# Kernel tuning notes

Hardware: AMD Instinct MI355X
Metric: run time of the kernel (lower is better)

## Reference

```python
import jax, jax.numpy as jnp
import numpy as np

B, FRAMES, NBINS, HOP = 4, 400, 129, 240
T = FRAMES * HOP  # 96000


def hann_window(K, dtype=jnp.float32):
    # torch.hann_window default is periodic=True: 0.5*(1 - cos(2*pi*n/K))
    n = jnp.arange(K, dtype=dtype)
    return 0.5 - 0.5 * jnp.cos(2.0 * jnp.pi * n / K)


def get_minimum_phase_fir(log_mag):
    # log_mag: [B, F, NBINS] -> full spectrum [B, F, N], N = 2*(NBINS-1)
    full = jnp.concatenate([log_mag, jnp.flip(log_mag, -1)[..., 1:-1]], axis=-1)
    N = full.shape[-1]
    # Hilbert transform (scipy-style analytic signal), N even
    Xf = jnp.fft.fft(full, axis=-1)
    h = jnp.concatenate([
        jnp.ones((1,), full.dtype),
        2.0 * jnp.ones((N // 2 - 1,), full.dtype),
        jnp.ones((1,), full.dtype),
        jnp.zeros((N // 2 - 1,), full.dtype),
    ])
    analytic = jnp.fft.ifft(Xf * h, axis=-1)
    min_phase = -jnp.imag(analytic)
    freq_resp = jnp.exp(full + 1j * min_phase)
    return jnp.real(jnp.fft.ifft(freq_resp, axis=-1))  # [B, F, N]


def windowing(kernel):
    K = kernel.shape[-1]
    w = hann_window(K, kernel.dtype)
    w = w.at[: K // 2].set(1.0)
    return kernel * w


def upsample_linear(x, scale):
    # x: [B, K, L] -> [B, K, L*scale], matches F.upsample(mode='linear', align_corners=False)
    L = x.shape[-1]
    out = jnp.arange(L * scale, dtype=x.dtype)
    src = jnp.clip((out + 0.5) / scale - 0.5, 0.0, L - 1.0)
    lo = jnp.floor(src).astype(jnp.int32)
    hi = jnp.minimum(lo + 1, L - 1)
    w = src - lo.astype(x.dtype)
    return x[..., lo] * (1.0 - w) + x[..., hi] * w


def fir_filt(x, h):
    # x: [B, T], h: [B, T, K]; causal time-varying FIR: y[t] = sum_k h[t,k] * x[t-k]
    K = h.shape[-1]
    Tn = x.shape[-1]
    x_pad = jnp.pad(x, ((0, 0), (K - 1, 0)))
    idx = jnp.arange(Tn)[:, None] + jnp.arange(K)[None, :]  # [T, K]
    frames = x_pad[:, idx]  # [B, T, K] (im2col-like gather)
    return jnp.einsum('btk,btk->bt', frames, jnp.flip(h, -1))


def setup_inputs() -> dict:
    key = jax.random.key(0)
    k1, k2 = jax.random.split(key)
    ex = jax.random.normal(k1, (B, T), dtype=jnp.float32)
    log_mag = jax.random.normal(k2, (B, FRAMES, NBINS), dtype=jnp.float32)
    return {"ex": ex, "log_mag": log_mag, "hop_length": HOP}


def reference(ex, log_mag, hop_length):
    kernel = get_minimum_phase_fir(log_mag)          # [B, F, K]
    kernel = windowing(kernel)
    up = upsample_linear(jnp.transpose(kernel, (0, 2, 1)), hop_length)  # [B, K, F*hop]
    up = jnp.transpose(up, (0, 2, 1))                # [B, F*hop, K]
    Tn = min(ex.shape[1], up.shape[1])
    ex = ex[:, :Tn]
    up = up[:, :Tn]
    return fir_filt(ex, up)
```

## Files before the change

kernel.cpp:

```cpp
#include <hip/hip_runtime.h>
#include <math.h>

#define NB 4
#define FRAMES 400
#define NBINS 129
#define HOP 240
#define T_LEN (FRAMES * HOP)
#define KLEN 256

#define REC_C { const float cn = fmaf(a2, cm, -cm1); cm1 = cm; cm = cn; }
#define REC_S { const float sn = fmaf(a2, sm, -sm1); sm1 = sm; sm = sn; }

__global__ __launch_bounds__(64) void gen_fir(const float* __restrict__ log_mag,
                                              float* __restrict__ kern) {
    const int bf = blockIdx.x;
    const int n  = threadIdx.x;

    __shared__ __align__(16) float  g[128];
    __shared__ __align__(16) float2 crci[128];

    const float* lm = log_mag + bf * NBINS;

    const float lmn0 = lm[n];
    const float lmn1 = lm[n + 64];

    const float rev_n = (float)n * (1.0f / 256.0f);
    const float ca = __builtin_amdgcn_cosf(rev_n);
    const float sa = __builtin_amdgcn_sinf(rev_n);
    const float a2  = 2.0f * ca;
    const float sgn = (n & 1) ? -1.0f : 1.0f;

    const float f0s  = lm[0];
    const float f128 = lm[128];

    {
        float cm1 = ca, cm = 1.0f, sm1 = -sa, sm = 0.0f;
        float U = 0.0f, V = 0.0f;
#pragma unroll
        for (int u = 0; u < 32; ++u) {
            float f;
            f = lm[4 * u + 0]; U = fmaf(f, cm, U); V = fmaf(f, cm, V);  REC_C; REC_S;
            f = lm[4 * u + 1]; U = fmaf(f, cm, U); V = fmaf(-f, sm, V); REC_C; REC_S;
            f = lm[4 * u + 2]; U = fmaf(f, cm, U); V = fmaf(-f, cm, V); REC_C; REC_S;
            f = lm[4 * u + 3]; U = fmaf(f, cm, U); V = fmaf(f, sm, V);  REC_C; REC_S;
        }
        const float base = -f0s + sgn * f128;
        g[n]      = (base + 2.0f * U) * (1.0f / 128.0f);
        g[n + 64] = (base + 2.0f * V) * (1.0f / 128.0f);
    }
    __syncthreads();

    {
        const float4* g4p = (const float4*)g;
        float cm1 = ca, cm = 1.0f, sm1 = -sa, sm = 0.0f;
        float U = 0.0f, V = 0.0f;
#pragma unroll
        for (int u = 0; u < 32; ++u) {
            const float4 gv = g4p[u];
            U = fmaf(gv.x, sm, U); V = fmaf(gv.x, sm, V);  REC_C; REC_S;
            U = fmaf(gv.y, sm, U); V = fmaf(gv.y, cm, V);  REC_C; REC_S;
            U = fmaf(gv.z, sm, U); V = fmaf(-gv.z, sm, V); REC_C; REC_S;
            U = fmaf(gv.w, sm, U); V = fmaf(-gv.w, cm, V); REC_C; REC_S;
        }
        const float mp0 = -U, mp1 = -V;
        const float e0 = __builtin_amdgcn_exp2f(lmn0 * 1.4426950408889634f);
        const float e1 = __builtin_amdgcn_exp2f(lmn1 * 1.4426950408889634f);
        float r0 = mp0 * 0.15915494309189535f; r0 -= floorf(r0);
        float r1 = mp1 * 0.15915494309189535f; r1 -= floorf(r1);
        const float w0 = (n == 0) ? 1.0f : 2.0f;
        crci[n]      = make_float2(w0 * e0 * __builtin_amdgcn_cosf(r0),
                                   w0 * e0 * __builtin_amdgcn_sinf(r0));
        crci[n + 64] = make_float2(2.0f * e1 * __builtin_amdgcn_cosf(r1),
                                   2.0f * e1 * __builtin_amdgcn_sinf(r1));
    }
    __syncthreads();

    {
        const float4* cc4 = (const float4*)crci;
        float cm1 = ca, cm = 1.0f, sm1 = -sa, sm = 0.0f;
        float W0 = 0.0f, W1 = 0.0f, W2 = 0.0f, W3 = 0.0f, X1 = 0.0f, X3 = 0.0f;
#pragma unroll
        for (int u = 0; u < 32; ++u) {
            const float4 q1 = cc4[2 * u];
            const float4 q2 = cc4[2 * u + 1];
            W0 = fmaf(q1.x, cm, W0); W0 = fmaf(-q1.y, sm, W0); REC_C; REC_S;
            W1 = fmaf(q1.z, cm, W1); W1 = fmaf(-q1.w, sm, W1);
            X1 = fmaf(q1.z, sm, X1); X1 = fmaf(q1.w, cm, X1);  REC_C; REC_S;
            W2 = fmaf(q2.x, cm, W2); W2 = fmaf(-q2.y, sm, W2); REC_C; REC_S;
            W3 = fmaf(q2.z, cm, W3); W3 = fmaf(-q2.w, sm, W3);
            X3 = fmaf(q2.z, sm, X3); X3 = fmaf(q2.w, cm, X3);  REC_C; REC_S;
        }
        const float e128 = __builtin_amdgcn_exp2f(f128 * 1.4426950408889634f);
        const float base = sgn * e128;
        const float s = 1.0f / 256.0f;
        float* kp = kern + bf * KLEN;
        kp[n]       = (W0 + W1 + W2 + W3 + base) * s;
        kp[n + 64]  = (W0 - X1 - W2 + X3 + base) * s;
        kp[n + 128] = (W0 - W1 + W2 - W3 + base) * s * (0.5f + 0.5f * ca);
        kp[n + 192] = (W0 + X1 - W2 - X3 + base) * s * (0.5f - 0.5f * sa);
    }
}

__global__ __launch_bounds__(128) void fir_apply(const float* __restrict__ ex,
                                                 const float* __restrict__ kern,
                                                 float* __restrict__ out) {
    const int b   = blockIdx.y;
    const int bs  = blockIdx.x;
    const int tid = threadIdx.x;

    const int start = (bs == 0) ? 0 : 240 * bs - 120;
    const int end   = min(T_LEN, 240 * bs + 120);
    const int f     = (bs == 0) ? 0 : bs - 1;
    const int fh    = min(f + 1, FRAMES - 1);

    __shared__ float xs[496];

    const float* xb = ex + b * T_LEN;
    for (int i = tid; i < 496; i += 128) {
        const int t = start - 255 + i;
        xs[i] = (t >= 0 && t < T_LEN) ? xb[t] : 0.0f;
    }
    __syncthreads();

    const int te = start + 2 * tid;
    if (te >= end) return;

    float se = ((float)te + 0.5f) * (1.0f / HOP) - 0.5f;
    se = fminf(fmaxf(se, 0.0f), (float)(FRAMES - 1));
    float so = ((float)te + 1.5f) * (1.0f / HOP) - 0.5f;
    so = fminf(fmaxf(so, 0.0f), (float)(FRAMES - 1));
    const float we = se - (float)f;
    const float wo = so - (float)f;

    const float* kL = kern + (b * FRAMES + f)  * KLEN;
    const float* kH = kern + (b * FRAMES + fh) * KLEN;

    const int base = 2 * tid;
    float carry = xs[base + 256];
    float aeL = 0.0f, aeH = 0.0f, aoL = 0.0f, aoH = 0.0f;
#pragma unroll 4
    for (int u = 0; u < 64; ++u) {
        const float2 v1 = *(const float2*)&xs[base + 254 - 4 * u];
        const float2 v0 = *(const float2*)&xs[base + 252 - 4 * u];
        const float4 kl4 = *(const float4*)(kL + 4 * u);
        const float4 kh4 = *(const float4*)(kH + 4 * u);
        aeL = fmaf(v1.y,  kl4.x, aeL); aeH = fmaf(v1.y,  kh4.x, aeH);
        aoL = fmaf(carry, kl4.x, aoL); aoH = fmaf(carry, kh4.x, aoH);
        aeL = fmaf(v1.x,  kl4.y, aeL); aeH = fmaf(v1.x,  kh4.y, aeH);
        aoL = fmaf(v1.y,  kl4.y, aoL); aoH = fmaf(v1.y,  kh4.y, aoH);
        aeL = fmaf(v0.y,  kl4.z, aeL); aeH = fmaf(v0.y,  kh4.z, aeH);
        aoL = fmaf(v1.x,  kl4.z, aoL); aoH = fmaf(v1.x,  kh4.z, aoH);
        aeL = fmaf(v0.x,  kl4.w, aeL); aeH = fmaf(v0.x,  kh4.w, aeH);
        aoL = fmaf(v0.y,  kl4.w, aoL); aoH = fmaf(v0.y,  kh4.w, aoH);
        carry = v0.x;
    }

    const float y0 = aeL + we * (aeH - aeL);
    const float y1 = aoL + wo * (aoH - aoL);
    *(float2*)(out + b * T_LEN + te) = make_float2(y0, y1);
}

extern "C" void kernel_launch(void* const* d_in, const int* in_sizes, int n_in,
                              void* d_out, int out_size, void* d_ws, size_t ws_size,
                              hipStream_t stream) {
    const float* ex      = (const float*)d_in[0];
    const float* log_mag = (const float*)d_in[1];
    float* kern = (float*)d_ws;
    float* out  = (float*)d_out;

    gen_fir<<<NB * FRAMES, 64, 0, stream>>>(log_mag, kern);

    dim3 grid(401, NB);
    fir_apply<<<grid, 128, 0, stream>>>(ex, kern, out);
}
```

Baseline: 27.23 us.

## Fuse FIR generation into FIR apply kernel, computing two frame kernels per block

Merges the minimum-phase FIR generation kernel into the filtering kernel. Each 128-thread block now has its two waves each compute one frame's 256-tap kernel into shared memory, then applies the filter from shared memory. This removes the second launch and the global workspace round trip for kernels, but every frame's kernel is computed about twice, since adjacent blocks share frames. It also drops the intra-wave syncthreads and relies on single-wave execution for the LDS hand-off between stages.

```diff
diff --git a/kernel.cpp b/kernel.cpp
--- a/kernel.cpp
+++ b/kernel.cpp
@@ -8,50 +8,71 @@
 #define T_LEN (FRAMES * HOP)
 #define KLEN 256
 
-#define REC_C { const float cn = fmaf(a2, cm, -cm1); cm1 = cm; cm = cn; }
-#define REC_S { const float sn = fmaf(a2, sm, -sm1); sm1 = sm; sm = sn; }
+#define REC_C { const float cn_ = fmaf(a2, cm, -cm1); cm1 = cm; cm = cn_; }
+#define REC_S { const float sn_ = fmaf(a2, sm, -sm1); sm1 = sm; sm = sn_; }
 
-__global__ __launch_bounds__(64) void gen_fir(const float* __restrict__ log_mag,
-                                              float* __restrict__ kern) {
-    const int bf = blockIdx.x;
-    const int n  = threadIdx.x;
+__global__ __launch_bounds__(128) void ltv_fused(const float* __restrict__ ex,
+                                                 const float* __restrict__ log_mag,
+                                                 float* __restrict__ out) {
+    const int b    = blockIdx.y;
+    const int bs   = blockIdx.x;
+    const int tid  = threadIdx.x;
+    const int wv   = tid >> 6;
+    const int lane = tid & 63;
 
-    __shared__ __align__(16) float  g[128];
-    __shared__ __align__(16) float2 crci[128];
+    const int start = (bs == 0) ? 0 : 240 * bs - 120;
+    const int end   = min(T_LEN, 240 * bs + 120);
+    const int f     = (bs == 0) ? 0 : bs - 1;
+    const int fr    = min(f + wv, FRAMES - 1);
 
-    const float* lm = log_mag + bf * NBINS;
+    __shared__ __align__(16) float  lm01[2][132];
+    __shared__ __align__(16) float  g2[2][128];
+    __shared__ __align__(16) float2 crci2[2][128];
+    __shared__ __align__(16) float  kerL[256];
+    __shared__ __align__(16) float  kerH[256];
+    __shared__ __align__(16) float  xs[512];
 
-    const float lmn0 = lm[n];
-    const float lmn1 = lm[n + 64];
+    const float* xb = ex + b * T_LEN;
+    for (int i = tid; i < 496; i += 128) {
+        const int t = start - 255 + i;
+        xs[i] = (t >= 0 && t < T_LEN) ? xb[t] : 0.0f;
+    }
 
-    const float rev_n = (float)n * (1.0f / 256.0f);
+    const float* lmg = log_mag + (b * FRAMES + fr) * NBINS;
+    float* lmW = lm01[wv];
+    for (int i = lane; i < NBINS; i += 64) lmW[i] = lmg[i];
+
+    const float rev_n = (float)lane * (1.0f / 256.0f);
     const float ca = __builtin_amdgcn_cosf(rev_n);
     const float sa = __builtin_amdgcn_sinf(rev_n);
     const float a2  = 2.0f * ca;
-    const float sgn = (n & 1) ? -1.0f : 1.0f;
+    const float sgn = (lane & 1) ? -1.0f : 1.0f;
 
-    const float f0s  = lm[0];
-    const float f128 = lm[128];
+    float* gW = g2[wv];
+    float2* crciW = crci2[wv];
+
+    const float f0s  = lmW[0];
+    const float f128 = lmW[128];
 
     {
+        const float4* lmW4 = (const float4*)lmW;
         float cm1 = ca, cm = 1.0f, sm1 = -sa, sm = 0.0f;
         float U = 0.0f, V = 0.0f;
 #pragma unroll
         for (int u = 0; u < 32; ++u) {
-            float f;
-            f = lm[4 * u + 0]; U = fmaf(f, cm, U); V = fmaf(f, cm, V);  REC_C; REC_S;
-            f = lm[4 * u + 1]; U = fmaf(f, cm, U); V = fmaf(-f, sm, V); REC_C; REC_S;
-            f = lm[4 * u + 2]; U = fmaf(f, cm, U); V = fmaf(-f, cm, V); REC_C; REC_S;
-            f = lm[4 * u + 3]; U = fmaf(f, cm, U); V = fmaf(f, sm, V);  REC_C; REC_S;
+            const float4 f4 = lmW4[u];
+            U = fmaf(f4.x, cm, U); V = fmaf(f4.x, cm, V);  REC_C; REC_S;
+            U = fmaf(f4.y, cm, U); V = fmaf(-f4.y, sm, V); REC_C; REC_S;
+            U = fmaf(f4.z, cm, U); V = fmaf(-f4.z, cm, V); REC_C; REC_S;
+            U = fmaf(f4.w, cm, U); V = fmaf(f4.w, sm, V);  REC_C; REC_S;
         }
-        const float base = -f0s + sgn * f128;
-        g[n]      = (base + 2.0f * U) * (1.0f / 128.0f);
-        g[n + 64] = (base + 2.0f * V) * (1.0f / 128.0f);
+        const float base0 = -f0s + sgn * f128;
+        gW[lane]      = (base0 + 2.0f * U) * (1.0f / 128.0f);
+        gW[lane + 64] = (base0 + 2.0f * V) * (1.0f / 128.0f);
     }
-    __syncthreads();
 
     {
-        const float4* g4p = (const float4*)g;
+        const float4* g4p = (const float4*)gW;
         float cm1 = ca, cm = 1.0f, sm1 = -sa, sm = 0.0f;
         float U = 0.0f, V = 0.0f;
 #pragma unroll
@@ -63,20 +84,21 @@
             U = fmaf(gv.w, sm, U); V = fmaf(-gv.w, cm, V); REC_C; REC_S;
         }
         const float mp0 = -U, mp1 = -V;
+        const float lmn0 = lmW[lane];
+        const float lmn1 = lmW[lane + 64];
         const float e0 = __builtin_amdgcn_exp2f(lmn0 * 1.4426950408889634f);
         const float e1 = __builtin_amdgcn_exp2f(lmn1 * 1.4426950408889634f);
         float r0 = mp0 * 0.15915494309189535f; r0 -= floorf(r0);
         float r1 = mp1 * 0.15915494309189535f; r1 -= floorf(r1);
-        const float w0 = (n == 0) ? 1.0f : 2.0f;
-        crci[n]      = make_float2(w0 * e0 * __builtin_amdgcn_cosf(r0),
-                                   w0 * e0 * __builtin_amdgcn_sinf(r0));
-        crci[n + 64] = make_float2(2.0f * e1 * __builtin_amdgcn_cosf(r1),
-                                   2.0f * e1 * __builtin_amdgcn_sinf(r1));
+        const float w0 = (lane == 0) ? 1.0f : 2.0f;
+        crciW[lane]      = make_float2(w0 * e0 * __builtin_amdgcn_cosf(r0),
+                                       w0 * e0 * __builtin_amdgcn_sinf(r0));
+        crciW[lane + 64] = make_float2(2.0f * e1 * __builtin_amdgcn_cosf(r1),
+                                       2.0f * e1 * __builtin_amdgcn_sinf(r1));
     }
-    __syncthreads();
 
     {
-        const float4* cc4 = (const float4*)crci;
+        const float4* cc4 = (const float4*)crciW;
         float cm1 = ca, cm = 1.0f, sm1 = -sa, sm = 0.0f;
         float W0 = 0.0f, W1 = 0.0f, W2 = 0.0f, W3 = 0.0f, X1 = 0.0f, X3 = 0.0f;
 #pragma unroll
@@ -91,35 +113,15 @@
             X3 = fmaf(q2.z, sm, X3); X3 = fmaf(q2.w, cm, X3);  REC_C; REC_S;
         }
         const float e128 = __builtin_amdgcn_exp2f(f128 * 1.4426950408889634f);
-        const float base = sgn * e128;
+        const float base0 = sgn * e128;
         const float s = 1.0f / 256.0f;
-        float* kp = kern + bf * KLEN;
-        kp[n]       = (W0 + W1 + W2 + W3 + base) * s;
-        kp[n + 64]  = (W0 - X1 - W2 + X3 + base) * s;
-        kp[n + 128] = (W0 - W1 + W2 - W3 + base) * s * (0.5f + 0.5f * ca);
-        kp[n + 192] = (W0 + X1 - W2 - X3 + base) * s * (0.5f - 0.5f * sa);
+        float* kerW = wv ? kerH : kerL;
+        kerW[lane]       = (W0 + W1 + W2 + W3 + base0) * s;
+        kerW[lane + 64]  = (W0 - X1 - W2 + X3 + base0) * s;
+        kerW[lane + 128] = (W0 - W1 + W2 - W3 + base0) * s * (0.5f + 0.5f * ca);
+        kerW[lane + 192] = (W0 + X1 - W2 - X3 + base0) * s * (0.5f - 0.5f * sa);
     }
-}
 
-__global__ __launch_bounds__(128) void fir_apply(const float* __restrict__ ex,
-                                                 const float* __restrict__ kern,
-                                                 float* __restrict__ out) {
-    const int b   = blockIdx.y;
-    const int bs  = blockIdx.x;
-    const int tid = threadIdx.x;
-
-    const int start = (bs == 0) ? 0 : 240 * bs - 120;
-    const int end   = min(T_LEN, 240 * bs + 120);
-    const int f     = (bs == 0) ? 0 : bs - 1;
-    const int fh    = min(f + 1, FRAMES - 1);
-
-    __shared__ float xs[496];
-
-    const float* xb = ex + b * T_LEN;
-    for (int i = tid; i < 496; i += 128) {
-        const int t = start - 255 + i;
-        xs[i] = (t >= 0 && t < T_LEN) ? xb[t] : 0.0f;
-    }
     __syncthreads();
 
     const int te = start + 2 * tid;
@@ -132,8 +134,8 @@
     const float we = se - (float)f;
     const float wo = so - (float)f;
 
-    const float* kL = kern + (b * FRAMES + f)  * KLEN;
-    const float* kH = kern + (b * FRAMES + fh) * KLEN;
+    const float4* kL4 = (const float4*)kerL;
+    const float4* kH4 = (const float4*)kerH;
 
     const int base = 2 * tid;
     float carry = xs[base + 256];
@@ -142,8 +144,8 @@
     for (int u = 0; u < 64; ++u) {
         const float2 v1 = *(const float2*)&xs[base + 254 - 4 * u];
         const float2 v0 = *(const float2*)&xs[base + 252 - 4 * u];
-        const float4 kl4 = *(const float4*)(kL + 4 * u);
-        const float4 kh4 = *(const float4*)(kH + 4 * u);
+        const float4 kl4 = kL4[u];
+        const float4 kh4 = kH4[u];
         aeL = fmaf(v1.y,  kl4.x, aeL); aeH = fmaf(v1.y,  kh4.x, aeH);
         aoL = fmaf(carry, kl4.x, aoL); aoH = fmaf(carry, kh4.x, aoH);
         aeL = fmaf(v1.x,  kl4.y, aeL); aeH = fmaf(v1.x,  kh4.y, aeH);
@@ -165,11 +167,8 @@
                               hipStream_t stream) {
     const float* ex      = (const float*)d_in[0];
     const float* log_mag = (const float*)d_in[1];
-    float* kern = (float*)d_ws;
-    float* out  = (float*)d_out;
-
-    gen_fir<<<NB * FRAMES, 64, 0, stream>>>(log_mag, kern);
+    float* out = (float*)d_out;
 
     dim3 grid(401, NB);
-    fir_apply<<<grid, 128, 0, stream>>>(ex, kern, out);
+    ltv_fused<<<grid, 128, 0, stream>>>(ex, log_mag, out);
 }
```

Measured after the change: 38.63 us. 1.42x slower.
